# Kernel tuning notes

Hardware: AMD Instinct MI355X
Metric: run time of the kernel (lower is better)

The kernel has to match this reference:

```python
import jax, jax.numpy as jnp
import numpy as np

NUM_CLASSES = 19
EPS = 1e-8  # torch cosine_similarity eps


def setup_inputs() -> dict:
    key = jax.random.key(0)
    k1, k2 = jax.random.split(key)
    inputs = jax.random.normal(k1, (8, 256, 128, 128), dtype=jnp.float32)  # (B, D, H, W)
    targets = jax.random.randint(k2, (8, 128, 128), 0, NUM_CLASSES)        # (B, H, W)
    return {"inputs": inputs, "targets": targets}


def reference(inputs, targets):
    B, D, H, W = inputs.shape
    C = NUM_CLASSES
    # (N, D) pixel embeddings and (N,) labels
    feats = jnp.transpose(inputs, (0, 2, 3, 1)).reshape(-1, D)
    labels = targets.reshape(-1)

    # per-class centroids: sum of embeddings / max(count, 1)  (matches sum_pixel = max(mask.sum(), 1))
    counts = jax.ops.segment_sum(jnp.ones(labels.shape, jnp.float32), labels, num_segments=C)  # (C,)
    sums = jax.ops.segment_sum(feats, labels, num_segments=C)                                   # (C, D)
    centers = sums / jnp.maximum(counts, 1.0)[:, None]
    present = counts > 0  # classes absent from the batch are skipped in both loss terms

    # ---- sim_loss: sum over present classes of mean_{pixels of class i} (1 - cos(center_i, feat)) ----
    cen_px = centers[labels]                                   # (N, D)
    dot = jnp.sum(feats * cen_px, axis=1)
    n_f = jnp.sqrt(jnp.sum(feats * feats, axis=1))
    n_c = jnp.sqrt(jnp.sum(cen_px * cen_px, axis=1))
    cos_px = dot / jnp.maximum(n_f * n_c, EPS)
    per_class = jax.ops.segment_sum(1.0 - cos_px, labels, num_segments=C) / jnp.maximum(counts, 1.0)
    sim_loss = jnp.sum(jnp.where(present, per_class, 0.0))

    # ---- diff_loss: for each present i, mean_j over all C classes of
    #      (1 - cos(center_j, center_i)) if j == i else relu(cos(center_j, center_i)) ----
    n_cen = jnp.sqrt(jnp.sum(centers * centers, axis=1))       # (C,)
    S = (centers @ centers.T) / jnp.maximum(n_cen[:, None] * n_cen[None, :], EPS)  # (C, C)
    eye = jnp.eye(C, dtype=bool)
    per_pair = jnp.where(eye, 1.0 - S, jnp.maximum(S, 0.0))    # row i = losses vs class i
    per_i = jnp.mean(per_pair, axis=1)                          # mean reduction over C rows
    diff_loss = jnp.sum(jnp.where(present, per_i, 0.0))

    return jnp.reshape(diff_loss + sim_loss, (1,))  # torch returns a shape-(1,) tensor
```

## Files before the change

kernel.cpp:

```cpp
#include <hip/hip_runtime.h>
#include <math.h>

#define D_DIM 256
#define HW 16384
#define C 19
#define N_PX 131072
#define EPS 1e-8f

#define S_SUM 1048576.0f
#define IS_SUM (1.0f/1048576.0f)
#define S_NF  65536.0f
#define IS_NF (1.0f/65536.0f)
#define S_DOT 65536.0f
#define IS_DOT (1.0f/65536.0f)

#define OFF_SUMS_I   0
#define OFF_CNT_I    5120
#define OFF_NCEN_F   5632
#define OFF_CNT_F    6144
#define OFF_DIFF_F   6656
#define OFF_CEN_F    8192
#define OFF_NF_I     16384
#define OFF_DOT_I    147456
#define OFF_WSUM_F   278528
#define WS_WORDS     280576

__global__ void k0_zero(int* __restrict__ ws) {
    int i = blockIdx.x * blockDim.x + threadIdx.x;
    int stride = gridDim.x * blockDim.x;
    for (; i < WS_WORDS; i += stride) ws[i] = 0;
}

__global__ __launch_bounds__(256) void k1_sums(const float* __restrict__ in,
                                               const int* __restrict__ tgt,
                                               int* __restrict__ wsi) {
    __shared__ int s_sum[C * 33];
    __shared__ int s_cnt[C];
    const int tid = threadIdx.x;
    for (int i = tid; i < C * 33; i += 256) s_sum[i] = 0;
    if (tid < C) s_cnt[tid] = 0;
    __syncthreads();

    const int px0 = blockIdx.x << 10;
    const int b   = px0 >> 14;
    const int hw  = (px0 & (HW - 1)) + (tid << 2);
    const int d0  = blockIdx.y << 5;
    const int p   = px0 + (tid << 2);
    const int l0 = tgt[p], l1 = tgt[p + 1], l2 = tgt[p + 2], l3 = tgt[p + 3];
    if (blockIdx.y == 0) {
        atomicAdd(&s_cnt[l0], 1); atomicAdd(&s_cnt[l1], 1);
        atomicAdd(&s_cnt[l2], 1); atomicAdd(&s_cnt[l3], 1);
    }

    const float* base = in + (((size_t)(b * D_DIM + d0)) << 14) + hw;
    float nf0 = 0.f, nf1 = 0.f, nf2 = 0.f, nf3 = 0.f;
    #pragma unroll
    for (int g = 0; g < 4; ++g) {
        float4 v[8];
        #pragma unroll
        for (int j = 0; j < 8; ++j)
            v[j] = *(const float4*)(base + ((size_t)(g * 8 + j) << 14));
        #pragma unroll
        for (int j = 0; j < 8; ++j) {
            const int dd = g * 8 + j;
            nf0 += v[j].x * v[j].x; nf1 += v[j].y * v[j].y;
            nf2 += v[j].z * v[j].z; nf3 += v[j].w * v[j].w;
            atomicAdd(&s_sum[l0 * 33 + dd], __float2int_rn(v[j].x * S_SUM));
            atomicAdd(&s_sum[l1 * 33 + dd], __float2int_rn(v[j].y * S_SUM));
            atomicAdd(&s_sum[l2 * 33 + dd], __float2int_rn(v[j].z * S_SUM));
            atomicAdd(&s_sum[l3 * 33 + dd], __float2int_rn(v[j].w * S_SUM));
        }
    }
    atomicAdd(&wsi[OFF_NF_I + p],     __float2int_rn(nf0 * S_NF));
    atomicAdd(&wsi[OFF_NF_I + p + 1], __float2int_rn(nf1 * S_NF));
    atomicAdd(&wsi[OFF_NF_I + p + 2], __float2int_rn(nf2 * S_NF));
    atomicAdd(&wsi[OFF_NF_I + p + 3], __float2int_rn(nf3 * S_NF));

    __syncthreads();
    for (int i = tid; i < C * 32; i += 256) {
        int c = i >> 5, dd = i & 31;
        atomicAdd(&wsi[OFF_SUMS_I + c * D_DIM + d0 + dd], s_sum[c * 33 + dd]);
    }
    if (blockIdx.y == 0 && tid < C) atomicAdd(&wsi[OFF_CNT_I + tid], s_cnt[tid]);
}

__global__ __launch_bounds__(384) void k2_centers(int* __restrict__ wsi) {
    float* wsf = (float*)wsi;
    __shared__ float s_cen[C * 257];
    __shared__ float s_ncen[C];
    __shared__ float s_pair[C * C];
    __shared__ float s_red[C];
    const int tid = threadIdx.x;

    for (int i = tid; i < C * D_DIM; i += 384) {
        int c = i >> 8, d = i & 255;
        float cnt = (float)wsi[OFF_CNT_I + c];
        float cen = ((float)wsi[OFF_SUMS_I + i]) * IS_SUM / fmaxf(cnt, 1.f);
        wsf[OFF_CEN_F + i] = cen;
        s_cen[c * 257 + d] = cen;
    }
    __syncthreads();
    if (tid < C) {
        float nsq = 0.f;
        for (int d = 0; d < D_DIM; ++d) {
            float x = s_cen[tid * 257 + d];
            nsq += x * x;
        }
        float n = sqrtf(nsq);
        s_ncen[tid] = n;
        wsf[OFF_NCEN_F + tid] = n;
        wsf[OFF_CNT_F + tid]  = (float)wsi[OFF_CNT_I + tid];
    }
    __syncthreads();
    if (tid < C * C) {
        int i = tid / C, j = tid % C;
        float dot = 0.f;
        for (int d = 0; d < D_DIM; ++d)
            dot += s_cen[i * 257 + d] * s_cen[j * 257 + d];
        float S = dot / fmaxf(s_ncen[i] * s_ncen[j], EPS);
        s_pair[tid] = (i == j) ? (1.f - S) : fmaxf(S, 0.f);
    }
    __syncthreads();
    if (tid < C) {
        float row = 0.f;
        for (int j = 0; j < C; ++j) row += s_pair[tid * C + j];
        s_red[tid] = (wsi[OFF_CNT_I + tid] > 0) ? (row / (float)C) : 0.f;
    }
    __syncthreads();
    if (tid == 0) {
        float diff = 0.f;
        for (int i = 0; i < C; ++i) diff += s_red[i];
        wsf[OFF_DIFF_F] = diff;
    }
}

__global__ __launch_bounds__(256) void k3_dot(const float* __restrict__ in,
                                              const int* __restrict__ tgt,
                                              int* __restrict__ wsi) {
    const float* wsf = (const float*)wsi;
    __shared__ float s_cen[C * 33];
    const int tid = threadIdx.x;
    const int d0  = blockIdx.y << 5;
    for (int i = tid; i < C * 32; i += 256) {
        int c = i >> 5, dd = i & 31;
        s_cen[c * 33 + dd] = wsf[OFF_CEN_F + c * D_DIM + d0 + dd];
    }
    __syncthreads();

    const int px0 = blockIdx.x << 10;
    const int b   = px0 >> 14;
    const int hw  = (px0 & (HW - 1)) + (tid << 2);
    const int p   = px0 + (tid << 2);
    const int l0 = tgt[p], l1 = tgt[p + 1], l2 = tgt[p + 2], l3 = tgt[p + 3];

    const float* base = in + (((size_t)(b * D_DIM + d0)) << 14) + hw;
    float dt0 = 0.f, dt1 = 0.f, dt2 = 0.f, dt3 = 0.f;
    #pragma unroll
    for (int g = 0; g < 4; ++g) {
        float4 v[8];
        #pragma unroll
        for (int j = 0; j < 8; ++j)
            v[j] = *(const float4*)(base + ((size_t)(g * 8 + j) << 14));
        #pragma unroll
        for (int j = 0; j < 8; ++j) {
            const int dd = g * 8 + j;
            dt0 += v[j].x * s_cen[l0 * 33 + dd];
            dt1 += v[j].y * s_cen[l1 * 33 + dd];
            dt2 += v[j].z * s_cen[l2 * 33 + dd];
            dt3 += v[j].w * s_cen[l3 * 33 + dd];
        }
    }
    atomicAdd(&wsi[OFF_DOT_I + p],     __float2int_rn(dt0 * S_DOT));
    atomicAdd(&wsi[OFF_DOT_I + p + 1], __float2int_rn(dt1 * S_DOT));
    atomicAdd(&wsi[OFF_DOT_I + p + 2], __float2int_rn(dt2 * S_DOT));
    atomicAdd(&wsi[OFF_DOT_I + p + 3], __float2int_rn(dt3 * S_DOT));
}

__global__ __launch_bounds__(256) void k3b_sim(const int* __restrict__ tgt,
                                               int* __restrict__ wsi) {
    float* wsf = (float*)wsi;
    const int p = blockIdx.x * 256 + threadIdx.x;
    const int l = tgt[p];
    const float dot = (float)wsi[OFF_DOT_I + p] * IS_DOT;
    const float nf  = (float)wsi[OFF_NF_I + p]  * IS_NF;
    const float nc  = wsf[OFF_NCEN_F + l];
    const float cnt = wsf[OFF_CNT_F + l];
    const float cosv = dot / fmaxf(sqrtf(nf) * nc, EPS);
    float contrib = (1.f - cosv) / fmaxf(cnt, 1.f);
    #pragma unroll
    for (int off = 32; off > 0; off >>= 1)
        contrib += __shfl_down(contrib, off, 64);
    if ((threadIdx.x & 63) == 0)
        wsf[OFF_WSUM_F + blockIdx.x * 4 + (threadIdx.x >> 6)] = contrib;
}

__global__ __launch_bounds__(256) void k4_final(const int* __restrict__ wsi,
                                                float* __restrict__ out) {
    const float* wsf = (const float*)wsi;
    __shared__ float s_w[4];
    float s = 0.f;
    for (int k = threadIdx.x; k < 2048; k += 256) s += wsf[OFF_WSUM_F + k];
    #pragma unroll
    for (int off = 32; off > 0; off >>= 1)
        s += __shfl_down(s, off, 64);
    if ((threadIdx.x & 63) == 0) s_w[threadIdx.x >> 6] = s;
    __syncthreads();
    if (threadIdx.x == 0)
        out[0] = s_w[0] + s_w[1] + s_w[2] + s_w[3] + wsf[OFF_DIFF_F];
}

extern "C" void kernel_launch(void* const* d_in, const int* in_sizes, int n_in,
                              void* d_out, int out_size, void* d_ws, size_t ws_size,
                              hipStream_t stream) {
    const float* in  = (const float*)d_in[0];
    const int*   tgt = (const int*)d_in[1];
    float* out = (float*)d_out;
    int*   wsi = (int*)d_ws;

    k0_zero<<<512, 256, 0, stream>>>(wsi);
    k1_sums<<<dim3(128, 8), 256, 0, stream>>>(in, tgt, wsi);
    k2_centers<<<1, 384, 0, stream>>>(wsi);
    k3_dot<<<dim3(128, 8), 256, 0, stream>>>(in, tgt, wsi);
    k3b_sim<<<512, 256, 0, stream>>>(tgt, wsi);
    k4_final<<<1, 256, 0, stream>>>(wsi, out);
}
```

Measured before the change: 236.6 us.

## Fuse dot, norm and sim into one full-depth pass; drop per-pixel atomics

The second pass now loops over all 256 channels per pixel in a single kernel. It computes dot and feature norm in registers and reduces the cosine loss directly, replacing the split-D kernel with global integer atomics plus a separate sim kernel. Feature norms move out of the first pass, whose per-thread work shrinks to two pixels with twice the blocks, and the zeroing kernel now clears only the small accumulator area. This removes large per-pixel atomic traffic and a launch, at the cost of fewer, longer-running blocks in the fused pass (256 blocks), which may reduce memory-level parallelism.

```diff
diff --git a/kernel.cpp b/kernel.cpp
--- a/kernel.cpp
+++ b/kernel.cpp
@@ -9,26 +9,19 @@
 
 #define S_SUM 1048576.0f
 #define IS_SUM (1.0f/1048576.0f)
-#define S_NF  65536.0f
-#define IS_NF (1.0f/65536.0f)
-#define S_DOT 65536.0f
-#define IS_DOT (1.0f/65536.0f)
 
 #define OFF_SUMS_I   0
-#define OFF_CNT_I    5120
-#define OFF_NCEN_F   5632
-#define OFF_CNT_F    6144
-#define OFF_DIFF_F   6656
-#define OFF_CEN_F    8192
-#define OFF_NF_I     16384
-#define OFF_DOT_I    147456
-#define OFF_WSUM_F   278528
-#define WS_WORDS     280576
+#define OFF_CNT_I    4864
+#define OFF_DIFF_F   4883
+#define OFF_NCEN_F   4884
+#define OFF_ICNT_F   4903
+#define OFF_CEN_F    4928
+#define OFF_WSUM_F   9792
+#define WS_ZERO      4883
 
 __global__ void k0_zero(int* __restrict__ ws) {
     int i = blockIdx.x * blockDim.x + threadIdx.x;
-    int stride = gridDim.x * blockDim.x;
-    for (; i < WS_WORDS; i += stride) ws[i] = 0;
+    if (i < WS_ZERO) ws[i] = 0;
 }
 
 __global__ __launch_bounds__(256) void k1_sums(const float* __restrict__ in,
@@ -41,41 +34,30 @@
     if (tid < C) s_cnt[tid] = 0;
     __syncthreads();
 
-    const int px0 = blockIdx.x << 10;
+    const int px0 = blockIdx.x << 9;
     const int b   = px0 >> 14;
-    const int hw  = (px0 & (HW - 1)) + (tid << 2);
+    const int hw  = (px0 & (HW - 1)) + (tid << 1);
     const int d0  = blockIdx.y << 5;
-    const int p   = px0 + (tid << 2);
-    const int l0 = tgt[p], l1 = tgt[p + 1], l2 = tgt[p + 2], l3 = tgt[p + 3];
+    const int p   = px0 + (tid << 1);
+    const int la = tgt[p], lb = tgt[p + 1];
     if (blockIdx.y == 0) {
-        atomicAdd(&s_cnt[l0], 1); atomicAdd(&s_cnt[l1], 1);
-        atomicAdd(&s_cnt[l2], 1); atomicAdd(&s_cnt[l3], 1);
+        atomicAdd(&s_cnt[la], 1); atomicAdd(&s_cnt[lb], 1);
     }
 
     const float* base = in + (((size_t)(b * D_DIM + d0)) << 14) + hw;
-    float nf0 = 0.f, nf1 = 0.f, nf2 = 0.f, nf3 = 0.f;
     #pragma unroll
     for (int g = 0; g < 4; ++g) {
-        float4 v[8];
+        float2 v[8];
         #pragma unroll
         for (int j = 0; j < 8; ++j)
-            v[j] = *(const float4*)(base + ((size_t)(g * 8 + j) << 14));
+            v[j] = *(const float2*)(base + ((size_t)(g * 8 + j) << 14));
         #pragma unroll
         for (int j = 0; j < 8; ++j) {
             const int dd = g * 8 + j;
-            nf0 += v[j].x * v[j].x; nf1 += v[j].y * v[j].y;
-            nf2 += v[j].z * v[j].z; nf3 += v[j].w * v[j].w;
-            atomicAdd(&s_sum[l0 * 33 + dd], __float2int_rn(v[j].x * S_SUM));
-            atomicAdd(&s_sum[l1 * 33 + dd], __float2int_rn(v[j].y * S_SUM));
-            atomicAdd(&s_sum[l2 * 33 + dd], __float2int_rn(v[j].z * S_SUM));
-            atomicAdd(&s_sum[l3 * 33 + dd], __float2int_rn(v[j].w * S_SUM));
+            atomicAdd(&s_sum[la * 33 + dd], __float2int_rn(v[j].x * S_SUM));
+            atomicAdd(&s_sum[lb * 33 + dd], __float2int_rn(v[j].y * S_SUM));
         }
     }
-    atomicAdd(&wsi[OFF_NF_I + p],     __float2int_rn(nf0 * S_NF));
-    atomicAdd(&wsi[OFF_NF_I + p + 1], __float2int_rn(nf1 * S_NF));
-    atomicAdd(&wsi[OFF_NF_I + p + 2], __float2int_rn(nf2 * S_NF));
-    atomicAdd(&wsi[OFF_NF_I + p + 3], __float2int_rn(nf3 * S_NF));
-
     __syncthreads();
     for (int i = tid; i < C * 32; i += 256) {
         int c = i >> 5, dd = i & 31;
@@ -109,7 +91,8 @@
         float n = sqrtf(nsq);
         s_ncen[tid] = n;
         wsf[OFF_NCEN_F + tid] = n;
-        wsf[OFF_CNT_F + tid]  = (float)wsi[OFF_CNT_I + tid];
+        float cnt = (float)wsi[OFF_CNT_I + tid];
+        wsf[OFF_ICNT_F + tid] = 1.f / fmaxf(cnt, 1.f);
     }
     __syncthreads();
     if (tid < C * C) {
@@ -134,64 +117,61 @@
     }
 }
 
-__global__ __launch_bounds__(256) void k3_dot(const float* __restrict__ in,
+__global__ __launch_bounds__(256) void k3_sim(const float* __restrict__ in,
                                               const int* __restrict__ tgt,
                                               int* __restrict__ wsi) {
-    const float* wsf = (const float*)wsi;
-    __shared__ float s_cen[C * 33];
+    float* wsf = (float*)wsi;
+    __shared__ float4 s_cen4[C * 65];
+    __shared__ float s_ncen[C];
+    __shared__ float s_icnt[C];
     const int tid = threadIdx.x;
-    const int d0  = blockIdx.y << 5;
-    for (int i = tid; i < C * 32; i += 256) {
-        int c = i >> 5, dd = i & 31;
-        s_cen[c * 33 + dd] = wsf[OFF_CEN_F + c * D_DIM + d0 + dd];
-    }
-    __syncthreads();
-
-    const int px0 = blockIdx.x << 10;
+    const float4* cen_g = (const float4*)(wsf + OFF_CEN_F);
+    for (int i = tid; i < C * 64; i += 256) {
+        int c = i >> 6, g = i & 63;
+        s_cen4[c * 65 + g] = cen_g[c * 64 + g];
+    }
+    if (tid < C) {
+        s_ncen[tid] = wsf[OFF_NCEN_F + tid];
+        s_icnt[tid] = wsf[OFF_ICNT_F + tid];
+    }
+    __syncthreads();
+
+    const int px0 = blockIdx.x << 9;
     const int b   = px0 >> 14;
-    const int hw  = (px0 & (HW - 1)) + (tid << 2);
-    const int p   = px0 + (tid << 2);
-    const int l0 = tgt[p], l1 = tgt[p + 1], l2 = tgt[p + 2], l3 = tgt[p + 3];
-
-    const float* base = in + (((size_t)(b * D_DIM + d0)) << 14) + hw;
-    float dt0 = 0.f, dt1 = 0.f, dt2 = 0.f, dt3 = 0.f;
-    #pragma unroll
-    for (int g = 0; g < 4; ++g) {
-        float4 v[8];
+    const int hw  = (px0 & (HW - 1)) + (tid << 1);
+    const int p   = px0 + (tid << 1);
+    const int la = tgt[p], lb = tgt[p + 1];
+    const float4* ca = &s_cen4[la * 65];
+    const float4* cb = &s_cen4[lb * 65];
+
+    const float* base = in + (((size_t)(b * D_DIM)) << 14) + hw;
+    float dta = 0.f, dtb = 0.f, nfa = 0.f, nfb = 0.f;
+    #pragma unroll 4
+    for (int g = 0; g < 32; ++g) {
+        float2 v[8];
         #pragma unroll
         for (int j = 0; j < 8; ++j)
-            v[j] = *(const float4*)(base + ((size_t)(g * 8 + j) << 14));
-        #pragma unroll
-        for (int j = 0; j < 8; ++j) {
-            const int dd = g * 8 + j;
-            dt0 += v[j].x * s_cen[l0 * 33 + dd];
-            dt1 += v[j].y * s_cen[l1 * 33 + dd];
-            dt2 += v[j].z * s_cen[l2 * 33 + dd];
-            dt3 += v[j].w * s_cen[l3 * 33 + dd];
-        }
-    }
-    atomicAdd(&wsi[OFF_DOT_I + p],     __float2int_rn(dt0 * S_DOT));
-    atomicAdd(&wsi[OFF_DOT_I + p + 1], __float2int_rn(dt1 * S_DOT));
-    atomicAdd(&wsi[OFF_DOT_I + p + 2], __float2int_rn(dt2 * S_DOT));
-    atomicAdd(&wsi[OFF_DOT_I + p + 3], __float2int_rn(dt3 * S_DOT));
-}
-
-__global__ __launch_bounds__(256) void k3b_sim(const int* __restrict__ tgt,
-                                               int* __restrict__ wsi) {
-    float* wsf = (float*)wsi;
-    const int p = blockIdx.x * 256 + threadIdx.x;
-    const int l = tgt[p];
-    const float dot = (float)wsi[OFF_DOT_I + p] * IS_DOT;
-    const float nf  = (float)wsi[OFF_NF_I + p]  * IS_NF;
-    const float nc  = wsf[OFF_NCEN_F + l];
-    const float cnt = wsf[OFF_CNT_F + l];
-    const float cosv = dot / fmaxf(sqrtf(nf) * nc, EPS);
-    float contrib = (1.f - cosv) / fmaxf(cnt, 1.f);
+            v[j] = *(const float2*)(base + ((size_t)(g * 8 + j) << 14));
+        float4 a0 = ca[g * 2], a1 = ca[g * 2 + 1];
+        float4 b0 = cb[g * 2], b1 = cb[g * 2 + 1];
+        dta += v[0].x * a0.x + v[1].x * a0.y + v[2].x * a0.z + v[3].x * a0.w
+             + v[4].x * a1.x + v[5].x * a1.y + v[6].x * a1.z + v[7].x * a1.w;
+        dtb += v[0].y * b0.x + v[1].y * b0.y + v[2].y * b0.z + v[3].y * b0.w
+             + v[4].y * b1.x + v[5].y * b1.y + v[6].y * b1.z + v[7].y * b1.w;
+        nfa += v[0].x * v[0].x + v[1].x * v[1].x + v[2].x * v[2].x + v[3].x * v[3].x
+             + v[4].x * v[4].x + v[5].x * v[5].x + v[6].x * v[6].x + v[7].x * v[7].x;
+        nfb += v[0].y * v[0].y + v[1].y * v[1].y + v[2].y * v[2].y + v[3].y * v[3].y
+             + v[4].y * v[4].y + v[5].y * v[5].y + v[6].y * v[6].y + v[7].y * v[7].y;
+    }
+
+    const float cosa = dta / fmaxf(sqrtf(nfa) * s_ncen[la], EPS);
+    const float cosb = dtb / fmaxf(sqrtf(nfb) * s_ncen[lb], EPS);
+    float contrib = (1.f - cosa) * s_icnt[la] + (1.f - cosb) * s_icnt[lb];
     #pragma unroll
     for (int off = 32; off > 0; off >>= 1)
         contrib += __shfl_down(contrib, off, 64);
-    if ((threadIdx.x & 63) == 0)
-        wsf[OFF_WSUM_F + blockIdx.x * 4 + (threadIdx.x >> 6)] = contrib;
+    if ((tid & 63) == 0)
+        wsf[OFF_WSUM_F + blockIdx.x * 4 + (tid >> 6)] = contrib;
 }
 
 __global__ __launch_bounds__(256) void k4_final(const int* __restrict__ wsi,
@@ -199,7 +179,7 @@
     const float* wsf = (const float*)wsi;
     __shared__ float s_w[4];
     float s = 0.f;
-    for (int k = threadIdx.x; k < 2048; k += 256) s += wsf[OFF_WSUM_F + k];
+    for (int k = threadIdx.x; k < 1024; k += 256) s += wsf[OFF_WSUM_F + k];
     #pragma unroll
     for (int off = 32; off > 0; off >>= 1)
         s += __shfl_down(s, off, 64);
@@ -217,10 +197,9 @@
     float* out = (float*)d_out;
     int*   wsi = (int*)d_ws;
 
-    k0_zero<<<512, 256, 0, stream>>>(wsi);
-    k1_sums<<<dim3(128, 8), 256, 0, stream>>>(in, tgt, wsi);
+    k0_zero<<<20, 256, 0, stream>>>(wsi);
+    k1_sums<<<dim3(256, 8), 256, 0, stream>>>(in, tgt, wsi);
     k2_centers<<<1, 384, 0, stream>>>(wsi);
-    k3_dot<<<dim3(128, 8), 256, 0, stream>>>(in, tgt, wsi);
-    k3b_sim<<<512, 256, 0, stream>>>(tgt, wsi);
+    k3_sim<<<256, 256, 0, stream>>>(in, tgt, wsi);
     k4_final<<<1, 256, 0, stream>>>(wsi, out);
 }
```

After: 233.6 us. No clear change (-1.3%).
